# Kernel tuning notes

Measured on AMD Instinct MI355X. Metric: run time of the kernel, lower is better.

## Reference

```python
import jax, jax.numpy as jnp
import numpy as np
from jax import lax

SYM = 128
STATES = 2
T = 4194304


def setup_inputs() -> dict:
    key = jax.random.key(0)
    k_tok, k_ls, k_fin = jax.random.split(key, 3)
    tokens = jax.random.randint(k_tok, (T,), 0, SYM, dtype=jnp.int64 if jax.config.jax_enable_x64 else jnp.int32)
    # original init: ones / states / states; add noise so grads are non-degenerate
    ls = jnp.ones((SYM, STATES, STATES), dtype=jnp.float32) / (STATES * STATES)
    ls = ls + 0.01 * jax.random.normal(k_ls, (SYM, STATES, STATES), dtype=jnp.float32)
    final = jnp.ones((STATES, 1), dtype=jnp.float32)
    return {"tokens": tokens, "ls": ls, "final": final}


def reference(tokens, ls, final):
    # initial state vector [1, 0] (hardcoded in the original forward)
    states = ls.shape[1]
    v0 = jnp.zeros((states,), dtype=ls.dtype).at[0].set(1.0)

    def step(v, j):
        # gather the 2x2 transition for symbol j and advance: v <- v @ ls[j]
        return v @ ls[j], None

    v, _ = lax.scan(step, v0, tokens)
    # faithful to the original: the last token's matrix is applied a second time
    v = v @ ls[tokens[-1]]
    return v
```

## Files before the change

kernel.cpp:

```cpp
#include <hip/hip_runtime.h>


__device__ __forceinline__ float4 mm(const float4 A, const float4 B) {
    float4 C;
    C.x = fmaf(A.x, B.x, A.y * B.z);
    C.y = fmaf(A.x, B.y, A.y * B.w);
    C.z = fmaf(A.z, B.x, A.w * B.z);
    C.w = fmaf(A.z, B.y, A.w * B.w);
    return C;
}

__global__ __launch_bounds__(256) void scan_phase1(const int4* __restrict__ tok4,
                                                   const float4* __restrict__ ls,
                                                   float4* __restrict__ partials) {
    const int tid = threadIdx.x;
    const int gid = blockIdx.x * 256 + tid;

    const int4 t = tok4[gid];
    float4 m = ls[t.x];
    m = mm(m, ls[t.y]);
    m = mm(m, ls[t.z]);
    m = mm(m, ls[t.w]);

    __shared__ float4 sm[256];
    sm[tid] = m;
    __syncthreads();
    #pragma unroll
    for (int s = 128; s > 0; s >>= 1) {
        if (tid < s) sm[tid] = mm(sm[tid], sm[tid + s]);
        __syncthreads();
    }
    if (tid == 0) partials[blockIdx.x] = sm[0];
}

__global__ __launch_bounds__(256) void scan_phase2(const float4* __restrict__ partials,
                                                   const int* __restrict__ tokens,
                                                   const float4* __restrict__ ls,
                                                   float* __restrict__ out) {
    const int tid = threadIdx.x;
    float4 m = make_float4(1.f, 0.f, 0.f, 1.f);
    #pragma unroll
    for (int k = 0; k < 16; ++k)
        m = mm(m, partials[tid * 16 + k]);

    __shared__ float4 sm[256];
    sm[tid] = m;
    __syncthreads();
    #pragma unroll
    for (int s = 128; s > 0; s >>= 1) {
        if (tid < s) sm[tid] = mm(sm[tid], sm[tid + s]);
        __syncthreads();
    }
    if (tid == 0) {
        const float4 M = mm(sm[0], ls[tokens[4194304 - 1]]);
        out[0] = M.x;
        out[1] = M.y;
    }
}

extern "C" void kernel_launch(void* const* d_in, const int* in_sizes, int n_in,
                              void* d_out, int out_size, void* d_ws, size_t ws_size,
                              hipStream_t stream) {
    const int*    tokens = (const int*)d_in[0];
    const float4* ls     = (const float4*)d_in[1];
    float*  out      = (float*)d_out;
    float4* partials = (float4*)d_ws;

    scan_phase1<<<4096, 256, 0, stream>>>((const int4*)tokens, ls, partials);
    scan_phase2<<<1, 256, 0, stream>>>(partials, tokens, ls, out);
}
```

Before: 73.05 us.

## Double tokens per thread and replace shared-memory tree with wave shuffle reduction

Each phase-1 thread now multiplies 8 token matrices instead of 4, which halves the block count to 2048. Both phases reduce within each 64-lane wave using xor shuffles, with operand order chosen so the product stays non-commutative and ordered. Only the four per-wave results then go through shared memory, which removes eight barrier-separated LDS rounds. Each thread's serial dependency chain gets longer, and the per-wave reduction now does a matrix multiply on every lane at every step.

```diff
diff --git a/kernel.cpp b/kernel.cpp
--- a/kernel.cpp
+++ b/kernel.cpp
@@ -1,5 +1,10 @@
 #include <hip/hip_runtime.h>
 
+
+#define T_TOKENS 4194304
+#define TPB      256
+#define TOK_PER_THREAD 8
+#define BLOCKS   (T_TOKENS / (TPB * TOK_PER_THREAD))
 
 __device__ __forceinline__ float4 mm(const float4 A, const float4 B) {
     float4 C;
@@ -10,27 +15,44 @@
     return C;
 }
 
+__device__ __forceinline__ float4 wave_reduce_mm(float4 m, int lane) {
+    #pragma unroll
+    for (int s = 1; s < 64; s <<= 1) {
+        float4 o;
+        o.x = __shfl_xor(m.x, s, 64);
+        o.y = __shfl_xor(m.y, s, 64);
+        o.z = __shfl_xor(m.z, s, 64);
+        o.w = __shfl_xor(m.w, s, 64);
+        m = ((lane & s) == 0) ? mm(m, o) : mm(o, m);
+    }
+    return m;
+}
+
 __global__ __launch_bounds__(256) void scan_phase1(const int4* __restrict__ tok4,
                                                    const float4* __restrict__ ls,
                                                    float4* __restrict__ partials) {
     const int tid = threadIdx.x;
-    const int gid = blockIdx.x * 256 + tid;
+    const int g   = blockIdx.x * TPB + tid;
 
-    const int4 t = tok4[gid];
-    float4 m = ls[t.x];
-    m = mm(m, ls[t.y]);
-    m = mm(m, ls[t.z]);
-    m = mm(m, ls[t.w]);
+    const int4 a = tok4[2 * g];
+    const int4 b = tok4[2 * g + 1];
 
-    __shared__ float4 sm[256];
-    sm[tid] = m;
+    float4 m = ls[a.x];
+    m = mm(m, ls[a.y]);
+    m = mm(m, ls[a.z]);
+    m = mm(m, ls[a.w]);
+    m = mm(m, ls[b.x]);
+    m = mm(m, ls[b.y]);
+    m = mm(m, ls[b.z]);
+    m = mm(m, ls[b.w]);
+
+    m = wave_reduce_mm(m, tid & 63);
+
+    __shared__ float4 sm[4];
+    if ((tid & 63) == 0) sm[tid >> 6] = m;
     __syncthreads();
-    #pragma unroll
-    for (int s = 128; s > 0; s >>= 1) {
-        if (tid < s) sm[tid] = mm(sm[tid], sm[tid + s]);
-        __syncthreads();
-    }
-    if (tid == 0) partials[blockIdx.x] = sm[0];
+    if (tid == 0)
+        partials[blockIdx.x] = mm(mm(sm[0], sm[1]), mm(sm[2], sm[3]));
 }
 
 __global__ __launch_bounds__(256) void scan_phase2(const float4* __restrict__ partials,
@@ -38,21 +60,19 @@
                                                    const float4* __restrict__ ls,
                                                    float* __restrict__ out) {
     const int tid = threadIdx.x;
-    float4 m = make_float4(1.f, 0.f, 0.f, 1.f);
+    float4 m = partials[tid * 8];
     #pragma unroll
-    for (int k = 0; k < 16; ++k)
-        m = mm(m, partials[tid * 16 + k]);
+    for (int k = 1; k < 8; ++k)
+        m = mm(m, partials[tid * 8 + k]);
 
-    __shared__ float4 sm[256];
-    sm[tid] = m;
+    m = wave_reduce_mm(m, tid & 63);
+
+    __shared__ float4 sm[4];
+    if ((tid & 63) == 0) sm[tid >> 6] = m;
     __syncthreads();
-    #pragma unroll
-    for (int s = 128; s > 0; s >>= 1) {
-        if (tid < s) sm[tid] = mm(sm[tid], sm[tid + s]);
-        __syncthreads();
-    }
     if (tid == 0) {
-        const float4 M = mm(sm[0], ls[tokens[4194304 - 1]]);
+        float4 M = mm(mm(sm[0], sm[1]), mm(sm[2], sm[3]));
+        M = mm(M, ls[tokens[T_TOKENS - 1]]);
         out[0] = M.x;
         out[1] = M.y;
     }
@@ -66,6 +86,6 @@
     float*  out      = (float*)d_out;
     float4* partials = (float4*)d_ws;
 
-    scan_phase1<<<4096, 256, 0, stream>>>((const int4*)tokens, ls, partials);
-    scan_phase2<<<1, 256, 0, stream>>>(partials, tokens, ls, out);
+    scan_phase1<<<BLOCKS, TPB, 0, stream>>>((const int4*)tokens, ls, partials);
+    scan_phase2<<<1, TPB, 0, stream>>>(partials, tokens, ls, out);
 }
```

After: 71.82 us. Within noise of the previous version (-1.7%).
